# Performance work log

Measured on AMD Instinct MI355X. Metric: run time of the kernel, lower is better.

## Reference

```python
import jax, jax.numpy as jnp
import numpy as np

B, T, N, M = 8, 4, 1024, 4096
C_IN, C_ORIG = 256, 128
P1, P2 = 256, 256
EPS_D = 1e-8   # three_nn inverse-distance epsilon
EPS_BN = 1e-5  # torch BatchNorm1d default eps


def setup_inputs() -> dict:
    key = jax.random.key(0)
    ks = jax.random.split(key, 6)
    return {
        "xyzs": jax.random.normal(ks[0], (B, T, N, 3), dtype=jnp.float32),
        "original_xyzs": jax.random.normal(ks[1], (B, T, M, 3), dtype=jnp.float32),
        "features": jax.random.normal(ks[2], (B, T, C_IN, N), dtype=jnp.float32),
        "original_features": jax.random.normal(ks[3], (B, T, C_ORIG, M), dtype=jnp.float32),
        "W1": jax.random.normal(ks[4], (P1, C_IN + C_ORIG), dtype=jnp.float32) * 0.05,
        "gamma1": jnp.ones((P1,), jnp.float32),
        "beta1": jnp.zeros((P1,), jnp.float32),
        "W2": jax.random.normal(ks[5], (P2, P1), dtype=jnp.float32) * 0.05,
        "gamma2": jnp.ones((P2,), jnp.float32),
        "beta2": jnp.zeros((P2,), jnp.float32),
    }


def _three_nn_interpolate(xyzs, orig_xyzs, feats):
    # squared pairwise distances, as the pointnet2 three_nn kernel returns d^2
    # d2: [B,T,M,N]
    d2 = jnp.sum((orig_xyzs[:, :, :, None, :] - xyzs[:, :, None, :, :]) ** 2, axis=-1)
    neg, idx = jax.lax.top_k(-d2, 3)           # 3 nearest; idx: [B,T,M,3]
    dist = -neg
    w = 1.0 / (dist + EPS_D)
    w = w / jnp.sum(w, axis=-1, keepdims=True)  # [B,T,M,3]
    b, t, c, n = feats.shape
    m = idx.shape[2]
    # gather neighbor features: [B,T,C,M,3]
    g = jnp.take_along_axis(feats, idx.reshape(b, t, 1, m * 3), axis=3)
    g = g.reshape(b, t, c, m, 3)
    return jnp.einsum("btcmk,btmk->btcm", g, w)


def _bn_per_frame(x, gamma, beta):
    # torch training-mode BN applied per frame t: stats over (B, M) per (t, c)
    mean = jnp.mean(x, axis=(0, 3), keepdims=True)
    var = jnp.var(x, axis=(0, 3), keepdims=True)  # biased, matches torch normalization
    xh = (x - mean) * jax.lax.rsqrt(var + EPS_BN)
    return gamma[None, None, :, None] * xh + beta[None, None, :, None]


def reference(xyzs, original_xyzs, features, original_features,
              W1, gamma1, beta1, W2, gamma2, beta2):
    interp = _three_nn_interpolate(xyzs, original_xyzs, features)     # [B,T,C_IN,M]
    x = jnp.concatenate([interp, original_features], axis=2)          # [B,T,C_IN+C_ORIG,M]
    x = jnp.einsum("oc,btcm->btom", W1, x)                            # 1x1 conv, no bias
    x = jax.nn.relu(_bn_per_frame(x, gamma1, beta1))
    x = jnp.einsum("oc,btcm->btom", W2, x)
    x = jax.nn.relu(_bn_per_frame(x, gamma2, beta2))
    return original_xyzs, x
```

## Files before the change

kernel.cpp:

```cpp
#include <hip/hip_runtime.h>
#include <hip/hip_bf16.h>

#define Bb 8
#define Tt 4
#define Nn 1024
#define Mm 4096
#define BT 32
#define CIN 256
#define CORIG 128
#define CTOT 384
#define P1 256
#define P2 256
#define EPS_D 1e-8f
#define EPS_BN 1e-5f

typedef __attribute__((ext_vector_type(4))) float f32x4;
typedef __attribute__((ext_vector_type(8))) short s16x8;

__device__ __forceinline__ unsigned short f2bf(float f) {
    unsigned int u = __float_as_uint(f);
    unsigned int r = (u + 0x7FFFu + ((u >> 16) & 1u)) >> 16;
    return (unsigned short)r;
}
__device__ __forceinline__ float bf2f(unsigned short b) {
    return __uint_as_float((unsigned int)b << 16);
}
__device__ __forceinline__ void split_bf16(float f, unsigned short& h, unsigned short& l) {
    h = f2bf(f);
    l = f2bf(f - bf2f(h));
}

__global__ __launch_bounds__(256) void prep_w_kernel(
    const float* __restrict__ W, unsigned short* __restrict__ hi,
    unsigned short* __restrict__ lo, int total)
{
    int i = blockIdx.x * 256 + threadIdx.x;
    if (i < total) {
        unsigned short h, l;
        split_bf16(W[i], h, l);
        hi[i] = h; lo[i] = l;
    }
}

__global__ __launch_bounds__(256) void three_nn_kernel(
    const float* __restrict__ xyzs,
    const float* __restrict__ oxyzs,
    int*   __restrict__ idx_out,
    float* __restrict__ w_out)
{
    __shared__ float sx[Nn], sy[Nn], sz[Nn];
    int bt = blockIdx.y;
    const float* base = xyzs + (size_t)bt * Nn * 3;
    for (int i = threadIdx.x; i < Nn; i += 256) {
        sx[i] = base[i * 3 + 0];
        sy[i] = base[i * 3 + 1];
        sz[i] = base[i * 3 + 2];
    }
    __syncthreads();

    int m = blockIdx.x * 256 + threadIdx.x;
    size_t q = ((size_t)bt * Mm + m) * 3;
    float qx = oxyzs[q + 0], qy = oxyzs[q + 1], qz = oxyzs[q + 2];

    float d0 = 3.4e38f, d1 = 3.4e38f, d2v = 3.4e38f;
    int   i0 = 0, i1 = 0, i2 = 0;
    #pragma unroll 4
    for (int n = 0; n < Nn; n++) {
        float dx = qx - sx[n], dy = qy - sy[n], dz = qz - sz[n];
        float d = dx * dx + dy * dy + dz * dz;
        bool lt0 = d < d0, lt1 = d < d1, lt2 = d < d2v;
        i2  = lt1 ? i1 : (lt2 ? n : i2);
        d2v = lt1 ? d1 : (lt2 ? d : d2v);
        i1  = lt0 ? i0 : (lt1 ? n : i1);
        d1  = lt0 ? d0 : (lt1 ? d : d1);
        i0  = lt0 ? n : i0;
        d0  = lt0 ? d : d0;
    }
    float w0 = 1.0f / (d0 + EPS_D);
    float w1 = 1.0f / (d1 + EPS_D);
    float w2 = 1.0f / (d2v + EPS_D);
    float inv = 1.0f / (w0 + w1 + w2);
    idx_out[q + 0] = i0; idx_out[q + 1] = i1; idx_out[q + 2] = i2;
    w_out[q + 0] = w0 * inv; w_out[q + 1] = w1 * inv; w_out[q + 2] = w2 * inv;
}

__global__ __launch_bounds__(256) void interp_concat_kernel(
    const float* __restrict__ feats,
    const float* __restrict__ ofeats,
    const int*   __restrict__ idx,
    const float* __restrict__ w,
    float* __restrict__ X)
{
    int bt = blockIdx.y;
    int c  = blockIdx.x >> 4;
    int m  = ((blockIdx.x & 15) << 8) | threadIdx.x;
    size_t xoff = ((size_t)bt * CTOT + c) * Mm + m;
    if (c < CIN) {
        size_t iw = ((size_t)bt * Mm + m) * 3;
        int   j0 = idx[iw + 0], j1 = idx[iw + 1], j2 = idx[iw + 2];
        float w0 = w[iw + 0],   w1 = w[iw + 1],   w2 = w[iw + 2];
        const float* frow = feats + ((size_t)bt * CIN + c) * Nn;
        X[xoff] = w0 * frow[j0] + w1 * frow[j1] + w2 * frow[j2];
    } else {
        X[xoff] = ofeats[((size_t)bt * CORIG + (c - CIN)) * Mm + m];
    }
}

template <int KTOT, bool TRANSFORM>
__global__ __launch_bounds__(256) void mfma_gemm_kernel(
    const unsigned short* __restrict__ Whi,
    const unsigned short* __restrict__ Wlo,
    const float* __restrict__ Xg,
    const float* __restrict__ stats,
    float* __restrict__ Y)
{
    __shared__ unsigned short sAhi[128][40];
    __shared__ unsigned short sAlo[128][40];
    __shared__ unsigned short sBhi[128][40];
    __shared__ unsigned short sBlo[128][40];

    const int tid = threadIdx.x;
    const int bt = blockIdx.z, t = bt & (Tt - 1);
    const int m0 = blockIdx.x * 128, o0 = blockIdx.y * 128;

    const int mo = tid & 127;
    const int kh = tid >> 7;
    const float* Xb = Xg + (size_t)bt * KTOT * Mm + m0 + mo;

    const int lane = tid & 63, wid = tid >> 6;
    const int wo = (wid >> 1) * 64, wm = (wid & 1) * 64;
    const int lr = lane & 15, kb = lane >> 4;

    f32x4 acc[4][4] = {};

    for (int k0 = 0; k0 < KTOT; k0 += 32) {
        {
            const uint4* ph = (const uint4*)&Whi[(size_t)(o0 + mo) * KTOT + k0 + kh * 16];
            const uint4* pl = (const uint4*)&Wlo[(size_t)(o0 + mo) * KTOT + k0 + kh * 16];
            uint4 h0 = ph[0], h1 = ph[1];
            uint4 l0 = pl[0], l1 = pl[1];
            *(uint4*)&sAhi[mo][kh * 16]     = h0;
            *(uint4*)&sAhi[mo][kh * 16 + 8] = h1;
            *(uint4*)&sAlo[mo][kh * 16]     = l0;
            *(uint4*)&sAlo[mo][kh * 16 + 8] = l1;
        }
        {
            float v[16];
            #pragma unroll
            for (int kk = 0; kk < 16; kk++)
                v[kk] = Xb[(size_t)(k0 + kh * 16 + kk) * Mm];
            if (TRANSFORM) {
                #pragma unroll
                for (int kk = 0; kk < 16; kk++) {
                    int k = k0 + kh * 16 + kk;
                    float a = stats[(t * KTOT + k) * 2 + 0];
                    float b = stats[(t * KTOT + k) * 2 + 1];
                    v[kk] = fmaxf(fmaf(a, v[kk], b), 0.0f);
                }
            }
            s16x8 H0, H1, L0, L1;
            #pragma unroll
            for (int kk = 0; kk < 8; kk++) {
                unsigned short h, l;
                split_bf16(v[kk], h, l);
                H0[kk] = (short)h; L0[kk] = (short)l;
                split_bf16(v[kk + 8], h, l);
                H1[kk] = (short)h; L1[kk] = (short)l;
            }
            *(s16x8*)&sBhi[mo][kh * 16]     = H0;
            *(s16x8*)&sBhi[mo][kh * 16 + 8] = H1;
            *(s16x8*)&sBlo[mo][kh * 16]     = L0;
            *(s16x8*)&sBlo[mo][kh * 16 + 8] = L1;
        }
        __syncthreads();

        s16x8 ah[4], al[4], bh[4], bl[4];
        #pragma unroll
        for (int f = 0; f < 4; f++) {
            ah[f] = *(const s16x8*)&sAhi[wo + f * 16 + lr][kb * 8];
            al[f] = *(const s16x8*)&sAlo[wo + f * 16 + lr][kb * 8];
            bh[f] = *(const s16x8*)&sBhi[wm + f * 16 + lr][kb * 8];
            bl[f] = *(const s16x8*)&sBlo[wm + f * 16 + lr][kb * 8];
        }
        #pragma unroll
        for (int fo = 0; fo < 4; fo++) {
            #pragma unroll
            for (int fn = 0; fn < 4; fn++) {
                acc[fo][fn] = __builtin_amdgcn_mfma_f32_16x16x32_bf16(ah[fo], bh[fn], acc[fo][fn], 0, 0, 0);
                acc[fo][fn] = __builtin_amdgcn_mfma_f32_16x16x32_bf16(ah[fo], bl[fn], acc[fo][fn], 0, 0, 0);
                acc[fo][fn] = __builtin_amdgcn_mfma_f32_16x16x32_bf16(al[fo], bh[fn], acc[fo][fn], 0, 0, 0);
            }
        }
        __syncthreads();
    }

    float* Yb = Y + (size_t)bt * 256 * Mm;
    #pragma unroll
    for (int fo = 0; fo < 4; fo++) {
        int obase = o0 + wo + fo * 16 + kb * 4;
        #pragma unroll
        for (int r = 0; r < 4; r++) {
            float* row = &Yb[(size_t)(obase + r) * Mm + m0 + wm + lr];
            #pragma unroll
            for (int fn = 0; fn < 4; fn++)
                row[fn * 16] = acc[fo][fn][r];
        }
    }
}

__global__ __launch_bounds__(256) void bn_stats_kernel(
    const float* __restrict__ Y,
    const float* __restrict__ gamma,
    const float* __restrict__ beta,
    float* __restrict__ stats)
{
    int o = blockIdx.x & 255;
    int t = blockIdx.x >> 8;
    int tid = threadIdx.x;
    float s1 = 0.0f, s2 = 0.0f;
    for (int b = 0; b < Bb; b++) {
        const float* row = Y + ((size_t)(b * Tt + t) * 256 + o) * Mm;
        for (int m = tid * 4; m < Mm; m += 1024) {
            float4 v = *(const float4*)&row[m];
            s1 += v.x + v.y + v.z + v.w;
            s2 += v.x * v.x + v.y * v.y + v.z * v.z + v.w * v.w;
        }
    }
    #pragma unroll
    for (int off = 32; off > 0; off >>= 1) {
        s1 += __shfl_down(s1, off);
        s2 += __shfl_down(s2, off);
    }
    __shared__ float r1[4], r2[4];
    int wv = tid >> 6;
    if ((tid & 63) == 0) { r1[wv] = s1; r2[wv] = s2; }
    __syncthreads();
    if (tid == 0) {
        float S1 = r1[0] + r1[1] + r1[2] + r1[3];
        float S2 = r2[0] + r2[1] + r2[2] + r2[3];
        const float inv = 1.0f / (float)(Bb * Mm);
        float mean = S1 * inv;
        float var  = S2 * inv - mean * mean;
        float a = gamma[o] * rsqrtf(var + EPS_BN);
        stats[(t * 256 + o) * 2 + 0] = a;
        stats[(t * 256 + o) * 2 + 1] = beta[o] - mean * a;
    }
}

__global__ __launch_bounds__(256) void bn_apply_kernel(
    const float* __restrict__ Y,
    const float* __restrict__ stats,
    float* __restrict__ out)
{
    size_t i4 = (size_t)blockIdx.x * 256 + threadIdx.x;
    size_t r = i4 >> 10;
    int o  = (int)(r & 255);
    int bt = (int)(r >> 8);
    int t  = bt & (Tt - 1);
    float a = stats[(t * 256 + o) * 2 + 0];
    float b = stats[(t * 256 + o) * 2 + 1];
    float4 v = *(const float4*)&Y[i4 * 4];
    v.x = fmaxf(fmaf(a, v.x, b), 0.0f);
    v.y = fmaxf(fmaf(a, v.y, b), 0.0f);
    v.z = fmaxf(fmaf(a, v.z, b), 0.0f);
    v.w = fmaxf(fmaf(a, v.w, b), 0.0f);
    *(float4*)&out[i4 * 4] = v;
}

extern "C" void kernel_launch(void* const* d_in, const int* in_sizes, int n_in,
                              void* d_out, int out_size, void* d_ws, size_t ws_size,
                              hipStream_t stream)
{
    const float* xyzs   = (const float*)d_in[0];
    const float* oxyzs  = (const float*)d_in[1];
    const float* feats  = (const float*)d_in[2];
    const float* ofeats = (const float*)d_in[3];
    const float* W1     = (const float*)d_in[4];
    const float* gamma1 = (const float*)d_in[5];
    const float* beta1  = (const float*)d_in[6];
    const float* W2     = (const float*)d_in[7];
    const float* gamma2 = (const float*)d_in[8];
    const float* beta2  = (const float*)d_in[9];
    float* out = (float*)d_out;

    char* ws = (char*)d_ws;
    int*            idx_ws = (int*)ws;
    float*          w_ws   = (float*)(ws + 1572864);
    unsigned short* Whi1   = (unsigned short*)(ws + 3145728);
    unsigned short* Wlo1   = (unsigned short*)(ws + 3342336);
    unsigned short* Whi2   = (unsigned short*)(ws + 3538944);
    unsigned short* Wlo2   = (unsigned short*)(ws + 3670016);
    float*          stats1 = (float*)(ws + 3801088);
    float*          stats2 = (float*)(ws + 3809280);
    float*          X      = (float*)(ws + 4194304);
    float*          Y1     = (float*)(ws + 4194304 + 201326592);
    float*          Y2     = X;

    hipMemcpyAsync(out, oxyzs, 393216 * sizeof(float),
                   hipMemcpyDeviceToDevice, stream);

    prep_w_kernel<<<(P1 * CTOT + 255) / 256, 256, 0, stream>>>(W1, Whi1, Wlo1, P1 * CTOT);
    prep_w_kernel<<<(P2 * P1 + 255) / 256, 256, 0, stream>>>(W2, Whi2, Wlo2, P2 * P1);

    three_nn_kernel<<<dim3(Mm / 256, BT), 256, 0, stream>>>(xyzs, oxyzs, idx_ws, w_ws);

    interp_concat_kernel<<<dim3(CTOT * (Mm / 256), BT), 256, 0, stream>>>(
        feats, ofeats, idx_ws, w_ws, X);

    mfma_gemm_kernel<CTOT, false><<<dim3(Mm / 128, 2, BT), 256, 0, stream>>>(
        Whi1, Wlo1, X, nullptr, Y1);

    bn_stats_kernel<<<Tt * 256, 256, 0, stream>>>(Y1, gamma1, beta1, stats1);

    mfma_gemm_kernel<P1, true><<<dim3(Mm / 128, 2, BT), 256, 0, stream>>>(
        Whi2, Wlo2, Y1, stats1, Y2);

    bn_stats_kernel<<<Tt * 256, 256, 0, stream>>>(Y2, gamma2, beta2, stats2);

    bn_apply_kernel<<<(BT * 256 * Mm / 4) / 256, 256, 0, stream>>>(
        Y2, stats2, out + 393216);
}
```

Baseline: 713.8 us.

## Transpose features for coalesced interpolation gather and fuse concat into GEMM

Features are first transposed to [bt][n][c] so the three-neighbor gather reads contiguous channel rows, and the interpolated values are staged in shared memory before coalesced float4 writes. The concat copy of original_features into X is removed; the first GEMM reads those rows directly from the input when k is at or past CIN. This removes uncoalesced gathers and a full copy pass, at the cost of an extra transpose kernel and its buffer traffic.

```diff
diff --git a/kernel.cpp b/kernel.cpp
--- a/kernel.cpp
+++ b/kernel.cpp
@@ -84,33 +84,75 @@
     w_out[q + 0] = w0 * inv; w_out[q + 1] = w1 * inv; w_out[q + 2] = w2 * inv;
 }
 
-__global__ __launch_bounds__(256) void interp_concat_kernel(
-    const float* __restrict__ feats,
-    const float* __restrict__ ofeats,
+__global__ __launch_bounds__(256) void transpose_feats_kernel(
+    const float* __restrict__ feats, float* __restrict__ featsT)
+{
+    __shared__ float tile[64][65];
+    int bt = blockIdx.z;
+    int n0 = blockIdx.x * 64;
+    int c0 = blockIdx.y * 64;
+    int tx = threadIdx.x & 63;
+    int ty = threadIdx.x >> 6;
+    const float* src = feats + ((size_t)bt * CIN + c0) * Nn + n0;
+    #pragma unroll
+    for (int r = 0; r < 16; r++) {
+        int c = ty + r * 4;
+        tile[c][tx] = src[(size_t)c * Nn + tx];
+    }
+    __syncthreads();
+    float* dst = featsT + ((size_t)bt * Nn + n0) * CIN + c0;
+    #pragma unroll
+    for (int r = 0; r < 16; r++) {
+        int n = ty + r * 4;
+        dst[(size_t)n * CIN + tx] = tile[tx][n];
+    }
+}
+
+__global__ __launch_bounds__(256) void interp_kernel(
+    const float* __restrict__ featsT,
     const int*   __restrict__ idx,
     const float* __restrict__ w,
-    float* __restrict__ X)
-{
+    float* __restrict__ Xi)
+{
+    __shared__ float sX[256][33];
+    __shared__ int   sidx[96];
+    __shared__ float swgt[96];
     int bt = blockIdx.y;
-    int c  = blockIdx.x >> 4;
-    int m  = ((blockIdx.x & 15) << 8) | threadIdx.x;
-    size_t xoff = ((size_t)bt * CTOT + c) * Mm + m;
-    if (c < CIN) {
-        size_t iw = ((size_t)bt * Mm + m) * 3;
-        int   j0 = idx[iw + 0], j1 = idx[iw + 1], j2 = idx[iw + 2];
-        float w0 = w[iw + 0],   w1 = w[iw + 1],   w2 = w[iw + 2];
-        const float* frow = feats + ((size_t)bt * CIN + c) * Nn;
-        X[xoff] = w0 * frow[j0] + w1 * frow[j1] + w2 * frow[j2];
-    } else {
-        X[xoff] = ofeats[((size_t)bt * CORIG + (c - CIN)) * Mm + m];
-    }
-}
-
-template <int KTOT, bool TRANSFORM>
+    int m0 = blockIdx.x * 32;
+    int tid = threadIdx.x;
+    size_t base = ((size_t)bt * Mm + m0) * 3;
+    if (tid < 96)       sidx[tid]      = idx[base + tid];
+    else if (tid < 192) swgt[tid - 96] = w[base + tid - 96];
+    __syncthreads();
+
+    const float* fb = featsT + (size_t)bt * Nn * CIN + tid;
+    #pragma unroll 4
+    for (int mm = 0; mm < 32; mm++) {
+        int   j0 = sidx[mm * 3 + 0], j1 = sidx[mm * 3 + 1], j2 = sidx[mm * 3 + 2];
+        float w0 = swgt[mm * 3 + 0], w1 = swgt[mm * 3 + 1], w2 = swgt[mm * 3 + 2];
+        sX[tid][mm] = w0 * fb[(size_t)j0 * CIN]
+                    + w1 * fb[(size_t)j1 * CIN]
+                    + w2 * fb[(size_t)j2 * CIN];
+    }
+    __syncthreads();
+
+    float* xb = Xi + (size_t)bt * CIN * Mm + m0;
+    #pragma unroll
+    for (int i = 0; i < 8; i++) {
+        int row = i * 32 + (tid >> 3);
+        int col = (tid & 7) * 4;
+        float4 v = make_float4(sX[row][col], sX[row][col + 1],
+                               sX[row][col + 2], sX[row][col + 3]);
+        *(float4*)&xb[(size_t)row * Mm + col] = v;
+    }
+}
+
+template <int KTOT, bool TRANSFORM, bool CONCAT>
 __global__ __launch_bounds__(256) void mfma_gemm_kernel(
     const unsigned short* __restrict__ Whi,
     const unsigned short* __restrict__ Wlo,
     const float* __restrict__ Xg,
+    const float* __restrict__ OF,
     const float* __restrict__ stats,
     float* __restrict__ Y)
 {
@@ -125,7 +167,8 @@
 
     const int mo = tid & 127;
     const int kh = tid >> 7;
-    const float* Xb = Xg + (size_t)bt * KTOT * Mm + m0 + mo;
+    const float* Xb  = Xg + (size_t)bt * (CONCAT ? CIN : KTOT) * Mm + m0 + mo;
+    const float* OFb = CONCAT ? (OF + (size_t)bt * CORIG * Mm + m0 + mo) : nullptr;
 
     const int lane = tid & 63, wid = tid >> 6;
     const int wo = (wid >> 1) * 64, wm = (wid & 1) * 64;
@@ -145,14 +188,18 @@
             *(uint4*)&sAlo[mo][kh * 16 + 8] = l1;
         }
         {
+            const int kg = k0 + kh * 16;
+            const float* bsrc = (CONCAT && kg >= CIN)
+                              ? (OFb + (size_t)(kg - CIN) * Mm)
+                              : (Xb + (size_t)kg * Mm);
             float v[16];
             #pragma unroll
             for (int kk = 0; kk < 16; kk++)
-                v[kk] = Xb[(size_t)(k0 + kh * 16 + kk) * Mm];
+                v[kk] = bsrc[(size_t)kk * Mm];
             if (TRANSFORM) {
                 #pragma unroll
                 for (int kk = 0; kk < 16; kk++) {
-                    int k = k0 + kh * 16 + kk;
+                    int k = kg + kk;
                     float a = stats[(t * KTOT + k) * 2 + 0];
                     float b = stats[(t * KTOT + k) * 2 + 1];
                     v[kk] = fmaxf(fmaf(a, v[kk], b), 0.0f);
@@ -292,9 +339,10 @@
     unsigned short* Wlo2   = (unsigned short*)(ws + 3670016);
     float*          stats1 = (float*)(ws + 3801088);
     float*          stats2 = (float*)(ws + 3809280);
-    float*          X      = (float*)(ws + 4194304);
-    float*          Y1     = (float*)(ws + 4194304 + 201326592);
-    float*          Y2     = X;
+    float*          featsT = (float*)(ws + 4194304);
+    float*          Xi     = (float*)(ws + 37748736);
+    float*          Y1     = (float*)(ws + 171966464);
+    float*          Y2     = Xi;
 
     hipMemcpyAsync(out, oxyzs, 393216 * sizeof(float),
                    hipMemcpyDeviceToDevice, stream);
@@ -304,16 +352,16 @@
 
     three_nn_kernel<<<dim3(Mm / 256, BT), 256, 0, stream>>>(xyzs, oxyzs, idx_ws, w_ws);
 
-    interp_concat_kernel<<<dim3(CTOT * (Mm / 256), BT), 256, 0, stream>>>(
-        feats, ofeats, idx_ws, w_ws, X);
-
-    mfma_gemm_kernel<CTOT, false><<<dim3(Mm / 128, 2, BT), 256, 0, stream>>>(
-        Whi1, Wlo1, X, nullptr, Y1);
+    transpose_feats_kernel<<<dim3(Nn / 64, CIN / 64, BT), 256, 0, stream>>>(feats, featsT);
+    interp_kernel<<<dim3(Mm / 32, BT), 256, 0, stream>>>(featsT, idx_ws, w_ws, Xi);
+
+    mfma_gemm_kernel<CTOT, false, true><<<dim3(Mm / 128, 2, BT), 256, 0, stream>>>(
+        Whi1, Wlo1, Xi, ofeats, nullptr, Y1);
 
     bn_stats_kernel<<<Tt * 256, 256, 0, stream>>>(Y1, gamma1, beta1, stats1);
 
-    mfma_gemm_kernel<P1, true><<<dim3(Mm / 128, 2, BT), 256, 0, stream>>>(
-        Whi2, Wlo2, Y1, stats1, Y2);
+    mfma_gemm_kernel<P1, true, false><<<dim3(Mm / 128, 2, BT), 256, 0, stream>>>(
+        Whi2, Wlo2, Y1, nullptr, stats1, Y2);
 
     bn_stats_kernel<<<Tt * 256, 256, 0, stream>>>(Y2, gamma2, beta2, stats2);
 
```

New measurement: 634.4 us. 11.1% less time.
